# Performance work log

Hardware: AMD Instinct MI355X
Metric: run time of the kernel (lower is better)

## Reference

```python
import jax, jax.numpy as jnp
import numpy as np

SIZE = 128
WIN = SIZE // 4   # sliding-window size == region size (32)
HALF = WIN // 2   # 16


def _conv(x, w, pad, groups=1):
    return jax.lax.conv_general_dilated(x, w, (1, 1), [(pad, pad), (pad, pad)],
        dimension_numbers=('NCHW', 'OIHW', 'NCHW'), feature_group_count=groups)


def _resize(x, h, w):
    # F.interpolate(..., mode='bilinear', align_corners=False)
    return jax.image.resize(x, (x.shape[0], x.shape[1], h, w), 'bilinear', antialias=False)


def _gauss_kernels():
    ax = np.linspace(-2.0, 2.0, 5)
    xx, yy = np.meshgrid(ax, ax)
    g = np.exp(-(xx ** 2 + yy ** 2) / 2.0) / (2.0 * np.pi)  # sigma = 1
    gx = (-xx * g).astype(np.float32)
    gy = (-yy * g).astype(np.float32)
    return (jnp.asarray(np.tile(gx[None, None], (3, 3, 1, 1))),
            jnp.asarray(np.tile(gy[None, None], (3, 3, 1, 1))))


def _edge_extract(x):
    Gx, Gy = _gauss_kernels()
    h = _conv(x, Gx, 2)
    v = _conv(x, Gy, 2)
    return jnp.tanh(jnp.sqrt(h * h + v * v + 1e-8))


def _color_moments(x, win=5):
    # F.unfold-based local mean / unbiased var / skewness, via depthwise box sums
    C = x.shape[1]
    n = float(win * win)
    ones = jnp.ones((C, 1, win, win), x.dtype)
    box = lambda z: _conv(z, ones, win // 2, groups=C)
    s1 = box(x); s2 = box(x * x); s3 = box(x * x * x)
    mean = s1 / n
    var = (s2 - n * mean * mean) / (n - 1.0)               # unbiased, matches torch.var
    m3 = (s3 - 3.0 * mean * s2 + 2.0 * n * mean ** 3) / n  # E[(x-m)^3]
    skew = m3 / (jnp.sqrt(jnp.maximum(var, 0.0)) ** 3 + 1e-6)
    return jnp.concatenate([mean, var, skew], 1)


def _locate_region(c):
    # scipy: gradient magnitude < 0.2 -> 4-connected label at argmax -> bbox center
    H, W = c.shape
    flat = jnp.argmax(c)
    xm = (flat // W).astype(jnp.int32)
    ym = (flat % W).astype(jnp.int32)
    gm = jnp.hypot(jnp.gradient(c, axis=0), jnp.gradient(c, axis=1))
    mask = gm < 0.2
    seed = jnp.zeros((H, W), bool).at[xm, ym].set(True) & mask

    def dil(r):
        d = r
        d = d | jnp.pad(r[1:, :], ((0, 1), (0, 0)))
        d = d | jnp.pad(r[:-1, :], ((1, 0), (0, 0)))
        d = d | jnp.pad(r[:, 1:], ((0, 0), (0, 1)))
        d = d | jnp.pad(r[:, :-1], ((0, 0), (1, 0)))
        return d & mask

    def body(s):
        r, _ = s
        nr = dil(r)
        return (nr, jnp.any(nr != r))

    region, _ = jax.lax.while_loop(lambda s: s[1], body, (seed, jnp.any(seed)))
    rows = jnp.any(region, 1); cols = jnp.any(region, 0)
    rs = jnp.argmax(rows); re = H - jnp.argmax(rows[::-1])
    cs = jnp.argmax(cols); ce = W - jnp.argmax(cols[::-1])
    ok = mask[xm, ym]  # label_at_max != 0
    x1 = jnp.where(ok, ((rs + re) // 2).astype(jnp.int32), xm)
    y1 = jnp.where(ok, ((cs + ce) // 2).astype(jnp.int32), ym)
    return x1, y1


def _affine_grid(move, H, W):
    # theta = [[1,0,tx],[0,1,ty]] with (tx,ty)=move, align_corners=False
    bx = (2.0 * jnp.arange(W, dtype=jnp.float32) + 1.0) / W - 1.0
    by = (2.0 * jnp.arange(H, dtype=jnp.float32) + 1.0) / H - 1.0
    gx = bx[None, None, :] + move[:, 0, None, None]
    gy = by[None, :, None] + move[:, 1, None, None]
    return jnp.stack(jnp.broadcast_arrays(gx, gy), -1)  # [B,H,W,2]


def _grid_sample(x, grid):
    # bilinear, zeros padding, align_corners=False (torch defaults)
    B, C, H, W = x.shape
    ix = ((grid[..., 0] + 1.0) * W - 1.0) / 2.0
    iy = ((grid[..., 1] + 1.0) * H - 1.0) / 2.0
    ix0 = jnp.floor(ix).astype(jnp.int32)
    iy0 = jnp.floor(iy).astype(jnp.int32)
    wx1 = ix - ix0; wy1 = iy - iy0
    b = jnp.arange(B)[:, None, None]

    def g(yy, xx):
        valid = ((xx >= 0) & (xx < W) & (yy >= 0) & (yy < H)).astype(x.dtype)
        v = x[b, :, jnp.clip(yy, 0, H - 1), jnp.clip(xx, 0, W - 1)]  # [B,Hg,Wg,C]
        return v * valid[..., None]

    out = (g(iy0, ix0) * ((1 - wy1) * (1 - wx1))[..., None]
         + g(iy0, ix0 + 1) * ((1 - wy1) * wx1)[..., None]
         + g(iy0 + 1, ix0) * (wy1 * (1 - wx1))[..., None]
         + g(iy0 + 1, ix0 + 1) * (wy1 * wx1)[..., None])
    return jnp.transpose(out, (0, 3, 1, 2))


def _bn_relu6(x, w, b):
    # BatchNorm2d in training mode (batch stats, biased var, eps=1e-5) + ReLU6
    m = x.mean((0, 2, 3), keepdims=True)
    v = ((x - m) ** 2).mean((0, 2, 3), keepdims=True)
    y = (x - m) / jnp.sqrt(v + 1e-5) * w[None, :, None, None] + b[None, :, None, None]
    return jnp.clip(y, 0.0, 6.0)


def setup_inputs():
    key = jax.random.key(0)
    ks = jax.random.split(key, 8)
    B, C = 8, 64
    return dict(
        warm_flag=1,
        feat1=jax.random.normal(ks[0], (B, C, SIZE, SIZE), jnp.float32),
        feat2=jax.random.normal(ks[1], (B, C, SIZE, SIZE), jnp.float32),
        cam1=jax.random.uniform(ks[2], (B, 64, 64), jnp.float32),
        cam2=jax.random.uniform(ks[3], (B, 64, 64), jnp.float32),
        f_g=jax.random.uniform(ks[4], (B, 3, 512, 512), jnp.float32),
        f_e=jax.random.uniform(ks[5], (B, 3, 512, 512), jnp.float32),
        conv1_w=jax.random.normal(ks[6], (C, 3, 3, 3), jnp.float32) * 0.1,
        conv1_b=jnp.zeros((C,), jnp.float32),
        conv2_w=jax.random.normal(ks[7], (C, 9, 3, 3), jnp.float32) * 0.1,
        conv2_b=jnp.zeros((C,), jnp.float32),
        bn_w=jnp.ones((C,), jnp.float32),
        bn_b=jnp.zeros((C,), jnp.float32),
    )


def reference(warm_flag, feat1, feat2, cam1, cam2, f_g, f_e,
              conv1_w, conv1_b, conv2_w, conv2_b, bn_w, bn_b):
    B = cam1.shape[0]
    c1 = _resize(cam1[:, None], SIZE, SIZE)
    c2 = _resize(cam2[:, None], SIZE, SIZE)

    if warm_flag == 1:
        # numpy/scipy path in torch is detached from autograd
        c1s = jax.lax.stop_gradient(c1)
        c2s = jax.lax.stop_gradient(c2)
        x1, y1 = jax.vmap(_locate_region)(c1s[:, 0])
        # valid-mode box convolution of cam2 with ones((H//4, W//4)), argmax
        box = jax.lax.conv_general_dilated(c2s, jnp.ones((1, 1, WIN, WIN), c2.dtype), (1, 1),
            'VALID', dimension_numbers=('NCHW', 'OIHW', 'NCHW'))[:, 0]
        Wv = box.shape[-1]
        flat = jnp.argmax(box.reshape(B, -1), -1)
        x2 = (flat // Wv + HALF).astype(jnp.int32)
        y2 = (flat % Wv + HALF).astype(jnp.int32)

        idx = jnp.arange(SIZE)
        def rect(xc, yc):
            r = (idx[None, :] >= jnp.maximum(xc - HALF, 0)[:, None]) & \
                (idx[None, :] < jnp.minimum(xc + HALF, SIZE)[:, None])
            cc = (idx[None, :] >= jnp.maximum(yc - HALF, 0)[:, None]) & \
                 (idx[None, :] < jnp.minimum(yc + HALF, SIZE)[:, None])
            return r[:, None, :, None] & cc[:, None, None, :]
        mask1 = rect(x1, y1).astype(feat1.dtype)
        mask2 = rect(x2, y2).astype(feat2.dtype)
        mi1 = jnp.stack([x1, y1], -1).astype(jnp.float32)
        mi2 = jnp.stack([x2, y2], -1).astype(jnp.float32)
    else:
        mask1 = jnp.zeros_like(feat1)
        mask2 = jnp.zeros_like(feat2)
        mi1 = jnp.zeros((B, 2), jnp.float32)
        mi2 = jnp.zeros((B, 2), jnp.float32)

    cam2_move = (mi2 - mi1) / (SIZE // 2)
    cam1_move = (mi1 - mi2) / (SIZE // 2)
    grid1 = _affine_grid(cam1_move, SIZE, SIZE)
    grid2 = _affine_grid(cam2_move, SIZE, SIZE)

    moments = _resize(_color_moments(f_e), SIZE, SIZE)   # [B,9,128,128]
    edge = _resize(_edge_extract(f_g), SIZE, SIZE)       # [B,3,128,128]
    feat1_edge = jnp.clip(_conv(edge, conv1_w, 1) + conv1_b[None, :, None, None], 0.0, 6.0)
    feat2_color = _conv(moments, conv2_w, 1) + conv2_b[None, :, None, None]

    feat2_move = _grid_sample(feat2_color * mask2, grid2)
    feat1_edge_move = _grid_sample(feat1_edge * mask1, grid1)

    Bc, C, H, W = feat1.shape
    f1 = feat1.reshape(Bc, C, -1)
    f2 = feat2.reshape(Bc, C, -1)
    f2m = feat2_move.reshape(Bc, C, -1)
    f1m = feat1_edge_move.reshape(Bc, C, -1)

    f2_attn = jax.nn.softmax(jnp.einsum('bcn,bdn->bcd', f2m, f1), -1)  # [B,C,C]
    feat1_apply = jnp.einsum('bcd,bdn->bcn', f2_attn, f1).reshape(Bc, C, H, W)
    f1_attn = jax.nn.softmax(jnp.einsum('bcn,bdn->bcd', f1m, f2), -1)
    feat2_apply = jnp.einsum('bcd,bdn->bcn', f1_attn, f2).reshape(Bc, C, H, W)

    feat1_apply = _bn_relu6(feat1_apply, bn_w, bn_b)
    feat2_apply = _bn_relu6(feat2_apply, bn_w, bn_b)

    if warm_flag == 0:
        return (feat1, feat2, grid1, grid2, feat1_edge, feat2_color, f1_attn, f2_attn, feat1, feat2)
    return (feat1_apply, feat2_apply, grid1, grid2, feat1_edge, feat2_color, f1_attn, f2_attn, feat1, feat2)
```

## Files before the change

### kernel.cpp

```cpp
#include <hip/hip_runtime.h>
#include <math.h>

#define SIZE 128
#define WIN 32
#define HALF 16
#define B 8
#define C 64
#define N (SIZE*SIZE)
#define BCN 8388608
#define BV 97

#define O_APPLY1   0
#define O_APPLY2   8388608
#define O_GRID1    16777216
#define O_GRID2    17039360
#define O_EDGEF    17301504
#define O_COLORF   25690112
#define O_ATTN1    34078720
#define O_ATTN2    34111488
#define O_FEAT1    34144256
#define O_FEAT2    42532864

#define WS_BNP     0
#define WS_XY      361472
#define WS_MOM     361600
#define WS_EDGE    1541248
#define WS_BN      1737856

#define NEGINF (-3.402823466e+38f)

typedef unsigned __int128 u128;

__device__ __forceinline__ u128 hfill(u128 g, u128 m) {
  u128 p = m;
  g |= p & (g << 1);  p &= p << 1;
  g |= p & (g << 2);  p &= p << 2;
  g |= p & (g << 4);  p &= p << 4;
  g |= p & (g << 8);  p &= p << 8;
  g |= p & (g << 16); p &= p << 16;
  g |= p & (g << 32); p &= p << 32;
  g |= p & (g << 64);
  p = m;
  g |= p & (g >> 1);  p &= p >> 1;
  g |= p & (g >> 2);  p &= p >> 2;
  g |= p & (g >> 4);  p &= p >> 4;
  g |= p & (g >> 8);  p &= p >> 8;
  g |= p & (g >> 16); p &= p >> 16;
  g |= p & (g >> 32); p &= p >> 32;
  g |= p & (g >> 64);
  return g;
}

__device__ __forceinline__ float resamp(const float* raw, int i, int j) {
  float fy = fminf(fmaxf(0.5f * (float)i - 0.25f, 0.f), 63.f);
  float fx = fminf(fmaxf(0.5f * (float)j - 0.25f, 0.f), 63.f);
  int y0 = (int)fy; float ty = fy - (float)y0; int y1i = min(y0 + 1, 63);
  int x0 = (int)fx; float tx = fx - (float)x0; int x1i = min(x0 + 1, 63);
  float a00 = raw[y0 * 64 + x0],  a01 = raw[y0 * 64 + x1i];
  float a10 = raw[y1i * 64 + x0], a11 = raw[y1i * 64 + x1i];
  return (1.f - ty) * ((1.f - tx) * a00 + tx * a01)
       + ty * ((1.f - tx) * a10 + tx * a11);
}

#define FRONT_B     8
#define NCHUNK      13
#define PREP_BASE   112
#define COPY_BASE   2160
#define COPY_BLKS   1024
#define STAGE1_GRID (COPY_BASE + 2 * COPY_BLKS)

__global__ __launch_bounds__(256, 3) void k_stage1(
    const float* __restrict__ cam1, const float* __restrict__ cam2,
    int* __restrict__ xy,
    const float* __restrict__ fe, const float* __restrict__ fg,
    float* __restrict__ mom, float* __restrict__ edge,
    const float4* __restrict__ f1, float4* __restrict__ o8,
    const float4* __restrict__ f2, float4* __restrict__ o9,
    float* __restrict__ pval, int* __restrict__ pidx) {
  __shared__ __align__(16) float smem[10752];
  int blk = blockIdx.x;
  int tid = threadIdx.x;

  if (blk >= COPY_BASE) {
    int c = blk - COPY_BASE;
    const float4* s; float4* d;
    if (c < COPY_BLKS) { s = f1; d = o8; }
    else               { s = f2; d = o9; c -= COPY_BLKS; }
    int base = c * 2048 + tid;
    float4 v0 = s[base];
    float4 v1 = s[base + 256];
    float4 v2 = s[base + 512];
    float4 v3 = s[base + 768];
    float4 v4 = s[base + 1024];
    float4 v5 = s[base + 1280];
    float4 v6 = s[base + 1536];
    float4 v7 = s[base + 1792];
    d[base]        = v0;
    d[base + 256]  = v1;
    d[base + 512]  = v2;
    d[base + 768]  = v3;
    d[base + 1024] = v4;
    d[base + 1280] = v5;
    d[base + 1536] = v6;
    d[base + 1792] = v7;
    return;
  }

  if (blk >= PREP_BASE) {
    float* sx = smem;
    int pblk = blk - PREP_BASE;
    if (pblk < 1536) {
      int tile = pblk & 63, ch = (pblk >> 6) % 3, b = pblk / 192;
      int ti0 = (tile >> 3) * 16, tj0 = (tile & 7) * 16;
      const float* src = fe + (size_t)(b * 3 + ch) * 262144;
      int oy0 = 4 * ti0 - 1, ox0 = 4 * tj0 - 1;
      for (int l = tid; l < 66 * 66; l += 256) {
        int r = l / 66, cc = l % 66;
        int gy = oy0 + r, gx = ox0 + cc;
        sx[l] = (gy >= 0 && gy < 512 && gx >= 0 && gx < 512) ? src[gy * 512 + gx] : 0.f;
      }
      __syncthreads();
      int ii = tid >> 4, jj = tid & 15;
      int i = ti0 + ii, j = tj0 + jj;
      float s1a[6], s2a[6], s3a[6], s1b[6], s2b[6], s3b[6];
      #pragma unroll
      for (int t = 0; t < 6; ++t) {
        float a1 = 0, a2 = 0, a3 = 0, b1 = 0, b2 = 0, b3 = 0;
        int lx = 4 * jj + t;
        #pragma unroll
        for (int r = 0; r < 6; ++r) {
          float v = sx[(4 * ii + r) * 66 + lx];
          float v2 = v * v, v3 = v2 * v;
          if (r < 5) { a1 += v; a2 += v2; a3 += v3; }
          if (r > 0) { b1 += v; b2 += v2; b3 += v3; }
        }
        s1a[t] = a1; s2a[t] = a2; s3a[t] = a3;
        s1b[t] = b1; s2b[t] = b2; s3b[t] = b3;
      }
      float am = 0, av = 0, as = 0;
      #pragma unroll
      for (int py = 0; py < 2; ++py) {
        #pragma unroll
        for (int px = 0; px < 2; ++px) {
          float s1 = 0, s2 = 0, s3 = 0;
          #pragma unroll
          for (int t = 0; t < 5; ++t) {
            s1 += py ? s1b[px + t] : s1a[px + t];
            s2 += py ? s2b[px + t] : s2a[px + t];
            s3 += py ? s3b[px + t] : s3a[px + t];
          }
          float mean = s1 / 25.f;
          float var  = (s2 - 25.f * mean * mean) / 24.f;
          float m3   = (s3 - 3.f * mean * s2 + 50.f * mean * mean * mean) / 25.f;
          float sq   = sqrtf(fmaxf(var, 0.f));
          float skew = m3 / (sq * sq * sq + 1e-6f);
          am += mean; av += var; as += skew;
        }
      }
      int base = (b * 9 + ch) * N + i * 128 + j;
      mom[base]         = 0.25f * am;
      mom[base + 3 * N] = 0.25f * av;
      mom[base + 6 * N] = 0.25f * as;
    } else {
      int eblk = pblk - 1536;
      int tile = eblk & 63, b = eblk >> 6;
      int ti0 = (tile >> 3) * 16, tj0 = (tile & 7) * 16;
      const float* s0 = fg + (size_t)b * 3 * 262144;
      int oy0 = 4 * ti0 - 1, ox0 = 4 * tj0 - 1;
      for (int l = tid; l < 66 * 66; l += 256) {
        int r = l / 66, cc = l % 66;
        int gy = oy0 + r, gx = ox0 + cc;
        float v = 0.f;
        if (gy >= 0 && gy < 512 && gx >= 0 && gx < 512) {
          int o = gy * 512 + gx;
          v = s0[o] + s0[262144 + o] + s0[524288 + o];
        }
        sx[l] = v;
      }
      __syncthreads();
      int ii = tid >> 4, jj = tid & 15;
      int i = ti0 + ii, j = tj0 + jj;
      const float INV2PI = 0.15915494309189535f;
      float wg[5], ug[5];
      #pragma unroll
      for (int t = 0; t < 5; ++t) {
        float a = (float)t - 2.f;
        float e = expf(-0.5f * a * a);
        wg[t] = e; ug[t] = -a * e;
      }
      float rAa[6], rAb[6], rBa[6], rBb[6];
      #pragma unroll
      for (int t = 0; t < 6; ++t) {
        float aa = 0, ab = 0, ba = 0, bb = 0;
        int lx = 4 * jj + t;
        #pragma unroll
        for (int r = 0; r < 6; ++r) {
          float v = sx[(4 * ii + r) * 66 + lx];
          if (r < 5) { aa += v * wg[r]; ba += v * ug[r]; }
          if (r > 0) { ab += v * wg[r - 1]; bb += v * ug[r - 1]; }
        }
        rAa[t] = aa; rAb[t] = ab; rBa[t] = ba; rBb[t] = bb;
      }
      float acc = 0.f;
      #pragma unroll
      for (int py = 0; py < 2; ++py) {
        #pragma unroll
        for (int px = 0; px < 2; ++px) {
          float h = 0, v = 0;
          #pragma unroll
          for (int t = 0; t < 5; ++t) {
            float A  = py ? rAb[px + t] : rAa[px + t];
            float Bw = py ? rBb[px + t] : rBa[px + t];
            h += A * ug[t];
            v += Bw * wg[t];
          }
          h *= INV2PI; v *= INV2PI;
          acc += tanhf(sqrtf(h * h + v * v + 1e-8f));
        }
      }
      edge[b * N + i * 128 + j] = 0.25f * acc;
    }
    return;
  }

  if (blk >= FRONT_B) {
    int cid = blk - FRONT_B;
    int b = cid / NCHUNK, chunk = cid % NCHUNK;
    int r0 = chunk * 8;
    int nr = min(8, BV - r0);
    int nrows = nr + WIN - 1;

    float* raw  = smem;
    float* rows = smem + 4096;
    float* csum = smem + 9216;
    float* sv   = smem + 10240;
    int*   si   = (int*)(smem + 10496);

    const float4* c4 = (const float4*)(cam2 + b * 4096);
    float4* r4 = (float4*)raw;
    #pragma unroll
    for (int k = 0; k < 4; ++k) r4[k * 256 + tid] = c4[k * 256 + tid];
    __syncthreads();

    for (int l = tid; l < nrows * 128; l += 256) {
      int q = l >> 7, c = l & 127;
      rows[l] = resamp(raw, r0 + q, c);
    }
    __syncthreads();

    for (int l = tid; l < nr * 128; l += 256) {
      int q = l >> 7, c = l & 127;
      float acc = 0.f;
      #pragma unroll
      for (int dy = 0; dy < WIN; ++dy) acc += rows[(q + dy) * 128 + c];
      csum[l] = acc;
    }
    __syncthreads();

    float bv = NEGINF; int bi = 0;
    for (int p = tid; p < nr * BV; p += 256) {
      int q = p / BV, cc = p % BV;
      float s = 0.f;
      #pragma unroll
      for (int dx = 0; dx < WIN; ++dx) s += csum[q * 128 + cc + dx];
      int gidx = (r0 + q) * BV + cc;
      if (s > bv || (s == bv && gidx < bi)) { bv = s; bi = gidx; }
    }
    sv[tid] = bv; si[tid] = bi;
    __syncthreads();
    for (int s = 128; s; s >>= 1) {
      if (tid < s) {
        float ov = sv[tid + s]; int oi = si[tid + s];
        if (ov > sv[tid] || (ov == sv[tid] && oi < si[tid])) { sv[tid] = ov; si[tid] = oi; }
      }
      __syncthreads();
    }
    if (tid == 0) { pval[b * NCHUNK + chunk] = sv[0]; pidx[b * NCHUNK + chunk] = si[0]; }
    return;
  }

  {
    int b = blk;
    float* raw = smem;
    float* sv  = smem + 4096;
    int*   si  = (int*)(smem + 4352);
    unsigned long long* mask64 = (unsigned long long*)(smem + 4608);
    int* sint = (int*)(smem + 5120);

    const float4* c4 = (const float4*)(cam1 + b * 4096);
    float4* r4 = (float4*)raw;
    #pragma unroll
    for (int k = 0; k < 4; ++k) r4[k * 256 + tid] = c4[k * 256 + tid];
    __syncthreads();

    float bv = NEGINF; int bi = 0;
    for (int k = 0; k < 64; ++k) {
      int pix = k * 256 + tid;
      float v1 = resamp(raw, pix >> 7, pix & 127);
      if (v1 > bv) { bv = v1; bi = pix; }
    }
    sv[tid] = bv; si[tid] = bi;
    __syncthreads();
    for (int s = 128; s; s >>= 1) {
      if (tid < s) {
        float ov = sv[tid + s]; int oi = si[tid + s];
        if (ov > sv[tid] || (ov == sv[tid] && oi < si[tid])) { sv[tid] = ov; si[tid] = oi; }
      }
      __syncthreads();
    }
    if (tid == 0) { sint[0] = si[0] >> 7; sint[1] = si[0] & 127; }
    __syncthreads();
    int s_xm = sint[0], s_ym = sint[1];

    for (int k = 0; k < 64; ++k) {
      int pix = k * 256 + tid;
      int i = pix >> 7, j = pix & 127;
      float gx_, gy_;
      if (i == 0)        gx_ = resamp(raw, 1, j) - resamp(raw, 0, j);
      else if (i == 127) gx_ = resamp(raw, 127, j) - resamp(raw, 126, j);
      else               gx_ = 0.5f * (resamp(raw, i + 1, j) - resamp(raw, i - 1, j));
      if (j == 0)        gy_ = resamp(raw, i, 1) - resamp(raw, i, 0);
      else if (j == 127) gy_ = resamp(raw, i, 127) - resamp(raw, i, 126);
      else               gy_ = 0.5f * (resamp(raw, i, j + 1) - resamp(raw, i, j - 1));
      bool pred = hypotf(gx_, gy_) < 0.2f;
      unsigned long long bal = __ballot(pred);
      if ((tid & 63) == 0) mask64[(i << 1) + (j >> 6)] = bal;
    }
    __syncthreads();
    if (tid == 0) {
      unsigned long long wdd = mask64[(s_xm << 1) + (s_ym >> 6)];
      sint[2] = (int)((wdd >> (s_ym & 63)) & 1ull);
    }
    __syncthreads();
    int s_ok = sint[2];

    if (tid < 64) {
      int l = tid;
      u128 m0 = ((u128)mask64[4 * l])     | ((u128)mask64[4 * l + 1] << 64);
      u128 m1 = ((u128)mask64[4 * l + 2]) | ((u128)mask64[4 * l + 3] << 64);
      u128 g0 = 0, g1v = 0;
      if (s_ok && (s_xm >> 1) == l) {
        if ((s_xm & 1) == 0) g0  = ((u128)1) << s_ym;
        else                 g1v = ((u128)1) << s_ym;
      }
      g0  = hfill(g0 & m0, m0);
      g1v = hfill(g1v & m1, m1);
      for (;;) {
        unsigned long long ulo = __shfl_up((unsigned long long)g1v, 1);
        unsigned long long uhi = __shfl_up((unsigned long long)(g1v >> 64), 1);
        u128 up = (l > 0) ? (((u128)ulo) | ((u128)uhi << 64)) : (u128)0;
        unsigned long long dlo = __shfl_down((unsigned long long)g0, 1);
        unsigned long long dhi = __shfl_down((unsigned long long)(g0 >> 64), 1);
        u128 dn = (l < 63) ? (((u128)dlo) | ((u128)dhi << 64)) : (u128)0;
        u128 n0 = hfill((g0 | up | g1v) & m0, m0);
        u128 n1 = hfill((g1v | n0 | dn) & m1, m1);
        bool chg = (n0 != g0) || (n1 != g1v);
        g0 = n0; g1v = n1;
        if (!__any(chg)) break;
      }
      unsigned long long be = __ballot(g0 != 0);
      unsigned long long bo = __ballot(g1v != 0);
      unsigned long long cl = (unsigned long long)(g0 | g1v);
      unsigned long long chh = (unsigned long long)((g0 | g1v) >> 64);
      for (int off = 32; off; off >>= 1) {
        cl  |= __shfl_xor(cl, off);
        chh |= __shfl_xor(chh, off);
      }
      if (l == 0) {
        int rs = 0, re = 0, cs_ = 0, ce = 0;
        if (be | bo) {
          int af = be ? (__ffsll(be) - 1) : 1000;
          int bf = bo ? (__ffsll(bo) - 1) : 1000;
          rs = min(af * 2, bf * 2 + 1);
          int al = be ? (63 - __clzll(be)) : -1000;
          int bl = bo ? (63 - __clzll(bo)) : -1000;
          re = max(al * 2, bl * 2 + 1) + 1;
          cs_ = cl ? (__ffsll(cl) - 1) : 64 + (__ffsll(chh) - 1);
          ce = chh ? 128 - __clzll(chh) : 64 - __clzll(cl);
        }
        int x1, y1;
        if (s_ok) { x1 = (rs + re) >> 1; y1 = (cs_ + ce) >> 1; }
        else      { x1 = s_xm;           y1 = s_ym; }
        xy[b] = x1; xy[8 + b] = y1;
      }
    }
  }
}

__global__ __launch_bounds__(256) void k_conv12(
    const float* __restrict__ edge, const float* __restrict__ w1,
    const float* __restrict__ b1, float* __restrict__ o4,
    const float* __restrict__ mom, const float* __restrict__ w2,
    const float* __restrict__ b2, float* __restrict__ o5,
    int* __restrict__ xy, float* __restrict__ g1, float* __restrict__ g2,
    const float* __restrict__ pval, const int* __restrict__ pidx) {
  __shared__ float tin[9 * 324];
  __shared__ float wsm[64 * 84];
  int tid = threadIdx.x;

  if (blockIdx.x >= 512) {
    if (blockIdx.y != 0) return;
    int b = blockIdx.x - 512;
    float bv = NEGINF; int bi = 0;
    for (int k = 0; k < NCHUNK; ++k) {
      float v = pval[b * NCHUNK + k]; int ix = pidx[b * NCHUNK + k];
      if (v > bv || (v == bv && ix < bi)) { bv = v; bi = ix; }
    }
    int x2i = bi / BV + HALF, y2i = bi % BV + HALF;
    if (tid == 0) { xy[16 + b] = x2i; xy[24 + b] = y2i; }
    float x1f = (float)xy[b], y1f = (float)xy[8 + b];
    float x2f = (float)x2i, y2f = (float)y2i;
    float m1x = (x1f - x2f) / 64.f, m1y = (y1f - y2f) / 64.f;
    float* g1b = g1 + (size_t)b * N * 2;
    float* g2b = g2 + (size_t)b * N * 2;
    for (int k = 0; k < 64; ++k) {
      int pix = k * 256 + tid;
      int h = pix >> 7, w = pix & 127;
      float bx = (2.f * (float)w + 1.f) / 128.f - 1.f;
      float by = (2.f * (float)h + 1.f) / 128.f - 1.f;
      g1b[pix * 2]     = bx + m1x; g1b[pix * 2 + 1] = by + m1y;
      g2b[pix * 2]     = bx - m1x; g2b[pix * 2 + 1] = by - m1y;
    }
    return;
  }

  int b = blockIdx.x >> 6, tile = blockIdx.x & 63;
  int ti0 = (tile >> 3) * 16, tj0 = (tile & 7) * 16;
  int i = tid >> 4, j = tid & 15;
  if (blockIdx.y == 0) {
    for (int l = tid; l < 324; l += 256) {
      int r = l / 18, cc = l % 18;
      int gi = ti0 + r - 1, gj = tj0 + cc - 1;
      tin[l] = (gi >= 0 && gi < 128 && gj >= 0 && gj < 128) ? edge[b * N + gi * 128 + gj] : 0.f;
    }
    for (int l = tid; l < 64 * 12; l += 256) {
      int o = l / 12, t = l % 12;
      wsm[l] = (t < 9) ? (w1[o * 27 + t] + w1[o * 27 + 9 + t] + w1[o * 27 + 18 + t]) : 0.f;
    }
    __syncthreads();
    float win[12];
    #pragma unroll
    for (int dy = 0; dy < 3; ++dy)
      #pragma unroll
      for (int dx = 0; dx < 3; ++dx)
        win[dy * 3 + dx] = tin[(i + dy) * 18 + (j + dx)];
    win[9] = 0.f; win[10] = 0.f; win[11] = 0.f;
    float* o = o4 + (size_t)b * C * N + (ti0 + i) * 128 + tj0 + j;
    for (int oc = 0; oc < C; ++oc) {
      const float4* wr = (const float4*)(wsm + oc * 12);
      float acc = b1[oc];
      #pragma unroll
      for (int q = 0; q < 3; ++q) {
        float4 w4 = wr[q];
        acc += w4.x * win[4 * q] + w4.y * win[4 * q + 1]
             + w4.z * win[4 * q + 2] + w4.w * win[4 * q + 3];
      }
      o[oc * N] = fminf(fmaxf(acc, 0.f), 6.f);
    }
  } else {
    for (int l = tid; l < 9 * 324; l += 256) {
      int ic = l / 324, rem = l % 324, r = rem / 18, cc = rem % 18;
      int gi = ti0 + r - 1, gj = tj0 + cc - 1;
      tin[l] = (gi >= 0 && gi < 128 && gj >= 0 && gj < 128) ? mom[(b * 9 + ic) * N + gi * 128 + gj] : 0.f;
    }
    for (int l = tid; l < 64 * 84; l += 256) {
      int o = l / 84, t = l % 84;
      wsm[l] = (t < 81) ? w2[o * 81 + t] : 0.f;
    }
    __syncthreads();
    float win[84];
    #pragma unroll
    for (int ic = 0; ic < 9; ++ic)
      #pragma unroll
      for (int dy = 0; dy < 3; ++dy)
        #pragma unroll
        for (int dx = 0; dx < 3; ++dx)
          win[ic * 9 + dy * 3 + dx] = tin[ic * 324 + (i + dy) * 18 + (j + dx)];
    win[81] = 0.f; win[82] = 0.f; win[83] = 0.f;
    float* o = o5 + (size_t)b * C * N + (ti0 + i) * 128 + tj0 + j;
    for (int oc = 0; oc < C; ++oc) {
      const float4* wr = (const float4*)(wsm + oc * 84);
      float acc = b2[oc];
      #pragma unroll
      for (int q = 0; q < 21; ++q) {
        float4 w4 = wr[q];
        acc += w4.x * win[4 * q] + w4.y * win[4 * q + 1]
             + w4.z * win[4 * q + 2] + w4.w * win[4 * q + 3];
      }
      o[oc * N] = acc;
    }
  }
}

__global__ __launch_bounds__(256) void k_logits(const float* __restrict__ aB1,
                                                const float* __restrict__ bB1,
                                                const float* __restrict__ aB2,
                                                const float* __restrict__ bB2,
                                                float* __restrict__ lg,
                                                const int* __restrict__ xy) {
  int mode = blockIdx.y;
  const float* aBase = mode ? aB2 : aB1;
  const float* bBase = mode ? bB2 : bB1;
  int b = blockIdx.x >> 4, sl = blockIdx.x & 15;
  int tid = threadIdx.x;
  int ci = (tid >> 4) << 2, di = (tid & 15) << 2;
  float* o = lg + (size_t)(((mode * 8 + b) * 16 + sl)) * 4096;

  int x1 = xy[b], y1 = xy[8 + b], x2 = xy[16 + b], y2 = xy[24 + b];
  int dyh, dxw, rlo, rhi, clo, chi;
  if (mode == 0) {
    dyh = y1 - y2; dxw = x1 - x2;
    rlo = max(x1 - HALF, 0); rhi = min(x1 + HALF, SIZE);
    clo = max(y1 - HALF, 0); chi = min(y1 + HALF, SIZE);
  } else {
    dyh = y2 - y1; dxw = x2 - x1;
    rlo = max(x2 - HALF, 0); rhi = min(x2 + HALF, SIZE);
    clo = max(y2 - HALF, 0); chi = min(y2 + HALF, SIZE);
  }
  int hlo = max(0, rlo - dyh), hhi = min(SIZE, rhi - dyh);
  int wlo = max(0, clo - dxw), whi = min(SIZE, chi - dxw);
  int wn = whi - wlo, hn = hhi - hlo;
  int npos = (wn > 0 && hn > 0) ? wn * hn : 0;
  if (sl * 64 >= npos) {
    #pragma unroll
    for (int u = 0; u < 4; ++u)
      #pragma unroll
      for (int v = 0; v < 4; ++v)
        o[(ci + u) * 64 + (di + v)] = 0.f;
    return;
  }

  __shared__ float aS[64][65];
  __shared__ float bS[64][65];
  const float* aB = aBase + (size_t)b * C * N;
  const float* bB = bBase + (size_t)b * C * N;
  for (int l = tid; l < 4096; l += 256) {
    int ch = l >> 6, k = l & 63;
    int p = sl * 64 + k;
    float av = 0.f, bv = 0.f;
    if (p < npos) {
      int h = hlo + p / wn, w = wlo + p % wn;
      av = aB[ch * N + (h + dyh) * 128 + (w + dxw)];
      bv = bB[ch * N + h * 128 + w];
    }
    aS[ch][k] = av; bS[ch][k] = bv;
  }
  __syncthreads();
  float acc[4][4] = {};
  #pragma unroll 4
  for (int k = 0; k < 64; ++k) {
    float a0 = aS[ci][k], a1 = aS[ci + 1][k], a2 = aS[ci + 2][k], a3 = aS[ci + 3][k];
    float b0 = bS[di][k], b1v = bS[di + 1][k], b2v = bS[di + 2][k], b3 = bS[di + 3][k];
    acc[0][0] += a0 * b0; acc[0][1] += a0 * b1v; acc[0][2] += a0 * b2v; acc[0][3] += a0 * b3;
    acc[1][0] += a1 * b0; acc[1][1] += a1 * b1v; acc[1][2] += a1 * b2v; acc[1][3] += a1 * b3;
    acc[2][0] += a2 * b0; acc[2][1] += a2 * b1v; acc[2][2] += a2 * b2v; acc[2][3] += a2 * b3;
    acc[3][0] += a3 * b0; acc[3][1] += a3 * b1v; acc[3][2] += a3 * b2v; acc[3][3] += a3 * b3;
  }
  #pragma unroll
  for (int u = 0; u < 4; ++u)
    #pragma unroll
    for (int v = 0; v < 4; ++v)
      o[(ci + u) * 64 + (di + v)] = acc[u][v];
}

__global__ void k_softmax(const float* __restrict__ lg,
                          float* __restrict__ o6, float* __restrict__ o7) {
  int row = blockIdx.x;
  int mode = blockIdx.y;
  float* dst = mode ? o7 : o6;
  int b = row >> 6, c = row & 63;
  int lane = threadIdx.x;
  const float* base = lg + (size_t)((mode * 8 + b) * 16) * 4096 + c * 64 + lane;
  float v = 0.f;
  #pragma unroll
  for (int sl = 0; sl < 16; ++sl) v += base[sl * 4096];
  float mx = v;
  for (int off = 32; off; off >>= 1) mx = fmaxf(mx, __shfl_xor(mx, off));
  float e = expf(v - mx);
  float s = e;
  for (int off = 32; off; off >>= 1) s += __shfl_xor(s, off);
  dst[row * 64 + lane] = e / s;
}

__global__ __launch_bounds__(256) void k_applyst(const float* __restrict__ a1,
                                                 const float* __restrict__ s1_,
                                                 float* __restrict__ d1,
                                                 const float* __restrict__ a2,
                                                 const float* __restrict__ s2_,
                                                 float* __restrict__ d2,
                                                 float* __restrict__ bnp) {
  const float* attn; const float* src; float* dst;
  int t = blockIdx.y;
  if (t == 0) { attn = a1; src = s1_; dst = d1; }
  else        { attn = a2; src = s2_; dst = d2; }
  int b = blockIdx.x >> 6, chunk = blockIdx.x & 63;
  int n0 = chunk * 256 + threadIdx.x;
  const float* s = src + (size_t)b * C * N + n0;
  float v[64];
  #pragma unroll
  for (int d = 0; d < 64; ++d) v[d] = s[d * N];
  const float4* at4 = (const float4*)(attn + b * 4096);
  float* o = dst + (size_t)b * C * N + n0;
  __shared__ float red[64][4], red2[64][4];
  int lane = threadIdx.x & 63, wave = threadIdx.x >> 6;
  for (int c = 0; c < 64; ++c) {
    float acc = 0.f;
    #pragma unroll
    for (int q = 0; q < 16; ++q) {
      float4 w4 = at4[c * 16 + q];
      acc += w4.x * v[4 * q] + w4.y * v[4 * q + 1] + w4.z * v[4 * q + 2] + w4.w * v[4 * q + 3];
    }
    o[c * N] = acc;
    float sr = acc, ssr = acc * acc;
    for (int off = 32; off; off >>= 1) {
      sr  += __shfl_xor(sr, off);
      ssr += __shfl_xor(ssr, off);
    }
    if (lane == 0) { red[c][wave] = sr; red2[c][wave] = ssr; }
  }
  __syncthreads();
  if (threadIdx.x < 64) {
    int c = threadIdx.x;
    float sr  = red[c][0] + red[c][1] + red[c][2] + red[c][3];
    float ssr = red2[c][0] + red2[c][1] + red2[c][2] + red2[c][3];
    int idx = (t * 64 + c) * 512 + blockIdx.x;
    bnp[idx]         = sr;
    bnp[65536 + idx] = ssr;
  }
}

__global__ void k_bnstats2(const float* __restrict__ bnp, float* __restrict__ stats) {
  __shared__ float sr[128][4], ssr[128][4];
  int tid = threadIdx.x;
  int combo = tid >> 2, q = tid & 3;
  float s = 0.f, ss = 0.f;
  for (int k = 0; k < 128; ++k) {
    int idx = combo * 512 + q * 128 + k;
    s  += bnp[idx];
    ss += bnp[65536 + idx];
  }
  sr[combo][q] = s; ssr[combo][q] = ss;
  __syncthreads();
  if (q == 0) {
    float S  = sr[combo][0] + sr[combo][1] + sr[combo][2] + sr[combo][3];
    float SS = ssr[combo][0] + ssr[combo][1] + ssr[combo][2] + ssr[combo][3];
    int t = combo >> 6, c = combo & 63;
    float mean = S / 131072.f;
    float var  = SS / 131072.f - mean * mean;
    stats[t * 128 + c]      = mean;
    stats[t * 128 + 64 + c] = 1.f / sqrtf(var + 1e-5f);
  }
}

__global__ __launch_bounds__(256) void k_bnapply(
    float4* __restrict__ o0, float4* __restrict__ o1,
    const float* __restrict__ stats,
    const float* __restrict__ bw, const float* __restrict__ bb) {
  int i = blockIdx.x * 256 + threadIdx.x;
  int t = blockIdx.y;
  float4* p = t ? o1 : o0;
  int c = (i >> 12) & 63;
  float m = stats[t * 128 + c], r = stats[t * 128 + 64 + c];
  float w_ = bw[c], b_ = bb[c];
  float4 v = p[i];
  v.x = fminf(fmaxf((v.x - m) * r * w_ + b_, 0.f), 6.f);
  v.y = fminf(fmaxf((v.y - m) * r * w_ + b_, 0.f), 6.f);
  v.z = fminf(fmaxf((v.z - m) * r * w_ + b_, 0.f), 6.f);
  v.w = fminf(fmaxf((v.w - m) * r * w_ + b_, 0.f), 6.f);
  p[i] = v;
}

extern "C" void kernel_launch(void* const* d_in, const int* in_sizes, int n_in,
                              void* d_out, int out_size, void* d_ws, size_t ws_size,
                              hipStream_t stream) {
  const float* feat1   = (const float*)d_in[1];
  const float* feat2   = (const float*)d_in[2];
  const float* cam1    = (const float*)d_in[3];
  const float* cam2    = (const float*)d_in[4];
  const float* f_g     = (const float*)d_in[5];
  const float* f_e     = (const float*)d_in[6];
  const float* conv1_w = (const float*)d_in[7];
  const float* conv1_b = (const float*)d_in[8];
  const float* conv2_w = (const float*)d_in[9];
  const float* conv2_b = (const float*)d_in[10];
  const float* bn_w    = (const float*)d_in[11];
  const float* bn_b    = (const float*)d_in[12];

  float* out = (float*)d_out;
  float* w = (float*)d_ws;
  int* xy = (int*)(w + WS_XY);
  float* pval = w + WS_BNP;
  int*   pidx = (int*)(w + WS_BNP + 128);

  float* o0 = out + O_APPLY1;
  float* o1 = out + O_APPLY2;
  float* o2 = out + O_GRID1;
  float* o3 = out + O_GRID2;
  float* o4 = out + O_EDGEF;
  float* o5 = out + O_COLORF;
  float* o6 = out + O_ATTN1;
  float* o7 = out + O_ATTN2;
  float* o8 = out + O_FEAT1;
  float* o9 = out + O_FEAT2;

  k_stage1<<<STAGE1_GRID, 256, 0, stream>>>(
      cam1, cam2, xy,
      f_e, f_g, w + WS_MOM, w + WS_EDGE,
      (const float4*)feat1, (float4*)o8, (const float4*)feat2, (float4*)o9,
      pval, pidx);

  k_conv12<<<dim3(520, 2), 256, 0, stream>>>(w + WS_EDGE, conv1_w, conv1_b, o4,
                                             w + WS_MOM, conv2_w, conv2_b, o5,
                                             xy, o2, o3, pval, pidx);

  k_logits<<<dim3(B * 16, 2), 256, 0, stream>>>(o4, feat2, o5, feat1,
                                                w + WS_MOM, xy);

  k_softmax<<<dim3(B * C, 2), 64, 0, stream>>>(w + WS_MOM, o6, o7);

  k_applyst<<<dim3(B * 64, 2), 256, 0, stream>>>(o7, feat1, o0, o6, feat2, o1,
                                                 w + WS_BNP);

  k_bnstats2<<<1, 512, 0, stream>>>(w + WS_BNP, w + WS_BN);

  k_bnapply<<<dim3(BCN / 4 / 256, 2), 256, 0, stream>>>(
      (float4*)o0, (float4*)o1, w + WS_BN, bn_w, bn_b);
}
```

Before: 536.3 us.

## Move feat copies into final BN kernel and keep column sums in registers

```diff
diff --git a/kernel.cpp b/kernel.cpp
--- a/kernel.cpp
+++ b/kernel.cpp
@@ -65,46 +65,17 @@
 #define FRONT_B     8
 #define NCHUNK      13
 #define PREP_BASE   112
-#define COPY_BASE   2160
-#define COPY_BLKS   1024
-#define STAGE1_GRID (COPY_BASE + 2 * COPY_BLKS)
-
-__global__ __launch_bounds__(256, 3) void k_stage1(
+#define STAGE1_GRID (PREP_BASE + 2048)
+
+__global__ __launch_bounds__(256, 4) void k_stage1(
     const float* __restrict__ cam1, const float* __restrict__ cam2,
     int* __restrict__ xy,
     const float* __restrict__ fe, const float* __restrict__ fg,
     float* __restrict__ mom, float* __restrict__ edge,
-    const float4* __restrict__ f1, float4* __restrict__ o8,
-    const float4* __restrict__ f2, float4* __restrict__ o9,
     float* __restrict__ pval, int* __restrict__ pidx) {
-  __shared__ __align__(16) float smem[10752];
+  __shared__ __align__(16) float smem[5632];
   int blk = blockIdx.x;
   int tid = threadIdx.x;
-
-  if (blk >= COPY_BASE) {
-    int c = blk - COPY_BASE;
-    const float4* s; float4* d;
-    if (c < COPY_BLKS) { s = f1; d = o8; }
-    else               { s = f2; d = o9; c -= COPY_BLKS; }
-    int base = c * 2048 + tid;
-    float4 v0 = s[base];
-    float4 v1 = s[base + 256];
-    float4 v2 = s[base + 512];
-    float4 v3 = s[base + 768];
-    float4 v4 = s[base + 1024];
-    float4 v5 = s[base + 1280];
-    float4 v6 = s[base + 1536];
-    float4 v7 = s[base + 1792];
-    d[base]        = v0;
-    d[base + 256]  = v1;
-    d[base + 512]  = v2;
-    d[base + 768]  = v3;
-    d[base + 1024] = v4;
-    d[base + 1280] = v5;
-    d[base + 1536] = v6;
-    d[base + 1792] = v7;
-    return;
-  }
 
   if (blk >= PREP_BASE) {
     float* sx = smem;
@@ -231,10 +202,9 @@
     int nrows = nr + WIN - 1;
 
     float* raw  = smem;
-    float* rows = smem + 4096;
-    float* csum = smem + 9216;
-    float* sv   = smem + 10240;
-    int*   si   = (int*)(smem + 10496);
+    float* csum = smem + 4096;
+    float* sv   = smem + 5120;
+    int*   si   = (int*)(smem + 5376);
 
     const float4* c4 = (const float4*)(cam2 + b * 4096);
     float4* r4 = (float4*)raw;
@@ -242,18 +212,21 @@
     for (int k = 0; k < 4; ++k) r4[k * 256 + tid] = c4[k * 256 + tid];
     __syncthreads();
 
-    for (int l = tid; l < nrows * 128; l += 256) {
-      int q = l >> 7, c = l & 127;
-      rows[l] = resamp(raw, r0 + q, c);
-    }
-    __syncthreads();
-
-    for (int l = tid; l < nr * 128; l += 256) {
-      int q = l >> 7, c = l & 127;
-      float acc = 0.f;
-      #pragma unroll
-      for (int dy = 0; dy < WIN; ++dy) acc += rows[(q + dy) * 128 + c];
-      csum[l] = acc;
+    if (tid < 128) {
+      int c = tid;
+      float vrow[39];
+      #pragma unroll
+      for (int q = 0; q < 39; ++q)
+        vrow[q] = (q < nrows) ? resamp(raw, r0 + q, c) : 0.f;
+      #pragma unroll
+      for (int q = 0; q < 8; ++q) {
+        if (q < nr) {
+          float acc = 0.f;
+          #pragma unroll
+          for (int dy = 0; dy < WIN; ++dy) acc += vrow[q + dy];
+          csum[q * 128 + c] = acc;
+        }
+      }
     }
     __syncthreads();
 
@@ -652,12 +625,15 @@
   }
 }
 
-__global__ __launch_bounds__(256) void k_bnapply(
+__global__ __launch_bounds__(256) void k_final(
+    const float4* __restrict__ f1, float4* __restrict__ o8,
+    const float4* __restrict__ f2, float4* __restrict__ o9,
     float4* __restrict__ o0, float4* __restrict__ o1,
     const float* __restrict__ stats,
     const float* __restrict__ bw, const float* __restrict__ bb) {
   int i = blockIdx.x * 256 + threadIdx.x;
   int t = blockIdx.y;
+  if (t == 0) o8[i] = f1[i]; else o9[i] = f2[i];
   float4* p = t ? o1 : o0;
   int c = (i >> 12) & 63;
   float m = stats[t * 128 + c], r = stats[t * 128 + 64 + c];
@@ -706,7 +682,6 @@
   k_stage1<<<STAGE1_GRID, 256, 0, stream>>>(
       cam1, cam2, xy,
       f_e, f_g, w + WS_MOM, w + WS_EDGE,
-      (const float4*)feat1, (float4*)o8, (const float4*)feat2, (float4*)o9,
       pval, pidx);
 
   k_conv12<<<dim3(520, 2), 256, 0, stream>>>(w + WS_EDGE, conv1_w, conv1_b, o4,
@@ -723,6 +698,7 @@
 
   k_bnstats2<<<1, 512, 0, stream>>>(w + WS_BNP, w + WS_BN);
 
-  k_bnapply<<<dim3(BCN / 4 / 256, 2), 256, 0, stream>>>(
+  k_final<<<dim3(BCN / 4 / 256, 2), 256, 0, stream>>>(
+      (const float4*)feat1, (float4*)o8, (const float4*)feat2, (float4*)o9,
       (float4*)o0, (float4*)o1, w + WS_BN, bn_w, bn_b);
 }
```

After: 572.3 us. 1.07x slower.
